# Kernel tuning notes

Hardware: AMD Instinct MI355X
Metric: run time of the kernel (lower is better)

## Reference

```python
import jax, jax.numpy as jnp
import numpy as np

B, Q, C, H, D, E, I = 8, 256, 192, 20, 64, 1500, 5120
HID = H * D  # 1280
EPS = 1e-5
SCALE = D ** -0.5


def _linear(x, w, b):
    return jnp.einsum('bsh,oh->bso', x, w) + b


def _layernorm(x, w, b):
    xf = x.astype(jnp.float32)
    mu = jnp.mean(xf, axis=-1, keepdims=True)
    var = jnp.mean(jnp.square(xf - mu), axis=-1, keepdims=True)
    return ((xf - mu) * jax.lax.rsqrt(var + EPS) * w + b).astype(x.dtype)


def _heads(x):  # [B,S,HID] -> [B,H,S,D]
    return x.reshape(B, -1, H, D).transpose(0, 2, 1, 3)


def setup_inputs() -> dict:
    key = jax.random.key(0)
    ks = jax.random.split(key, 24)
    s = 0.02
    inp = {
        'hidden_states': jax.random.normal(ks[0], (B, Q, HID), jnp.float32),
        'mask': jnp.zeros((B, 1, Q, Q + C), jnp.float32),
        'past_key': jax.random.normal(ks[1], (B, H, C, D), jnp.float32),
        'past_value': jax.random.normal(ks[2], (B, H, C, D), jnp.float32),
        'cross_key': jax.random.normal(ks[3], (B, H, E, D), jnp.float32),
        'cross_value': jax.random.normal(ks[4], (B, H, E, D), jnp.float32),
        'q_w': jax.random.normal(ks[5], (HID, HID), jnp.float32) * s,
        'q_b': jnp.zeros((HID,), jnp.float32),
        'k_w': jax.random.normal(ks[6], (HID, HID), jnp.float32) * s,
        'k_b': jnp.zeros((HID,), jnp.float32),
        'v_w': jax.random.normal(ks[7], (HID, HID), jnp.float32) * s,
        'v_b': jnp.zeros((HID,), jnp.float32),
        'o_w': jax.random.normal(ks[8], (HID, HID), jnp.float32) * s,
        'o_b': jnp.zeros((HID,), jnp.float32),
        'cq_w': jax.random.normal(ks[9], (HID, HID), jnp.float32) * s,
        'cq_b': jnp.zeros((HID,), jnp.float32),
        'co_w': jax.random.normal(ks[10], (HID, HID), jnp.float32) * s,
        'co_b': jnp.zeros((HID,), jnp.float32),
        'up_w': jax.random.normal(ks[11], (I, HID), jnp.float32) * s,
        'up_b': jnp.zeros((I,), jnp.float32),
        'down_w': jax.random.normal(ks[12], (HID, I), jnp.float32) * s,
        'down_b': jnp.zeros((HID,), jnp.float32),
        'ln1_w': jnp.ones((HID,), jnp.float32),
        'ln1_b': jnp.zeros((HID,), jnp.float32),
        'ln2_w': jnp.ones((HID,), jnp.float32),
        'ln2_b': jnp.zeros((HID,), jnp.float32),
        'ln3_w': jnp.ones((HID,), jnp.float32),
        'ln3_b': jnp.zeros((HID,), jnp.float32),
    }
    return inp


def reference(hidden_states, mask, past_key, past_value, cross_key, cross_value,
              q_w, q_b, k_w, k_b, v_w, v_b, o_w, o_b,
              cq_w, cq_b, co_w, co_b, up_w, up_b, down_w, down_b,
              ln1_w, ln1_b, ln2_w, ln2_b, ln3_w, ln3_b):
    # ---- self-attention block ----
    residual = hidden_states
    x = _layernorm(hidden_states, ln1_w, ln1_b)
    q = _heads(_linear(x, q_w, q_b) * SCALE)          # [B,H,Q,D]
    k_new = _heads(_linear(x, k_w, k_b))              # [B,H,Q,D]
    v_new = _heads(_linear(x, v_w, v_b))
    k = jnp.concatenate([past_key, k_new], axis=2)    # [B,H,C+Q,D]
    v = jnp.concatenate([past_value, v_new], axis=2)
    scores = jnp.einsum('bhqd,bhkd->bhqk', q, k) + mask
    attn = jnp.einsum('bhqk,bhkd->bhqd', jax.nn.softmax(scores, axis=-1), v)
    attn = attn.transpose(0, 2, 1, 3).reshape(B, Q, HID)
    attn_out = _linear(attn, o_w, o_b)
    present_key = k[:, :, Q:, :]
    present_value = v[:, :, Q:, :]
    h = residual + attn_out
    # ---- cross-attention block ----
    residual = h
    x = _layernorm(h, ln2_w, ln2_b)
    cq = _heads(_linear(x, cq_w, cq_b) * SCALE)       # [B,H,Q,D]
    cscores = jnp.einsum('bhqd,bhkd->bhqk', cq, cross_key)
    cattn = jnp.einsum('bhqk,bhkd->bhqd', jax.nn.softmax(cscores, axis=-1), cross_value)
    cattn = cattn.transpose(0, 2, 1, 3).reshape(B, Q, HID)
    h = residual + _linear(cattn, co_w, co_b)
    # ---- MLP block ----
    residual = h
    x = _layernorm(h, ln3_w, ln3_b)
    up = _linear(x, up_w, up_b)
    mlp_out = _linear(jax.nn.gelu(up, approximate=False), down_w, down_b)
    h = residual + mlp_out
    return (h, present_key, present_value)
```

## Files before the change

kernel.cpp:

```cpp
#include <hip/hip_runtime.h>
#include <math.h>

#define Bc   8
#define Qn   256
#define Cn   192
#define Hn   20
#define Dn   64
#define En   1500
#define In   5120
#define HIDn 1280
#define BQ   2048
#define KSELF 448
#define EPAD 1536
#define S1   (BQ*HIDn)
#define WSZ  (HIDn*HIDn)
#define BH   (Bc*Hn)

typedef __attribute__((ext_vector_type(8))) short bf16x8;
typedef __attribute__((ext_vector_type(4))) float f32x4;

__device__ __forceinline__ short f2bf(float f) {
  union { float f; unsigned u; } x; x.f = f;
  unsigned r = x.u + 0x7fffu + ((x.u >> 16) & 1u);
  return (short)(r >> 16);
}
__device__ __forceinline__ float bf2f(short s) {
  union { unsigned u; float f; } x; x.u = ((unsigned)(unsigned short)s) << 16;
  return x.f;
}
__device__ __forceinline__ void gload16(const short* g, short* l) {
  __builtin_amdgcn_global_load_lds(
      (const __attribute__((address_space(1))) void*)g,
      (__attribute__((address_space(3))) void*)l, 16, 0, 0);
}
__device__ __forceinline__ bf16x8 cvt8(const float* p) {
  const float4 a = *reinterpret_cast<const float4*>(p);
  const float4 b = *reinterpret_cast<const float4*>(p + 4);
  bf16x8 t;
  t[0] = f2bf(a.x); t[1] = f2bf(a.y); t[2] = f2bf(a.z); t[3] = f2bf(a.w);
  t[4] = f2bf(b.x); t[5] = f2bf(b.y); t[6] = f2bf(b.z); t[7] = f2bf(b.w);
  return t;
}

__global__ __launch_bounds__(256) void convert_all(
    const float* q, const float* k, const float* v, const float* o,
    const float* cq, const float* co, const float* up, const float* dn,
    short* wq, short* wk, short* wv, short* wo,
    short* wcq, short* wco, short* wup, short* wdn)
{
  const float* src; short* dst; int n;
  switch (blockIdx.y) {
    case 0: src = q;  dst = wq;  n = WSZ; break;
    case 1: src = k;  dst = wk;  n = WSZ; break;
    case 2: src = v;  dst = wv;  n = WSZ; break;
    case 3: src = o;  dst = wo;  n = WSZ; break;
    case 4: src = cq; dst = wcq; n = WSZ; break;
    case 5: src = co; dst = wco; n = WSZ; break;
    case 6: src = up; dst = wup; n = HIDn * In; break;
    default: src = dn; dst = wdn; n = HIDn * In; break;
  }
  const int i = (blockIdx.x * 256 + threadIdx.x) * 8;
  if (i >= n) return;
  *reinterpret_cast<bf16x8*>(dst + i) = cvt8(src + i);
}

__global__ __launch_bounds__(256) void prep_cross(
    const float* __restrict__ K, const float* __restrict__ V,
    short* __restrict__ Kc, short* __restrict__ Vc)
{
  const size_t idx = (size_t)blockIdx.x * 256 + threadIdx.x;
  const int d8 = (int)(idx & 7) * 8;
  const size_t t = idx >> 3;
  const int key = (int)(t % EPAD);
  const int bh  = (int)(t / EPAD);
  bf16x8 kv = (bf16x8)0, vv = (bf16x8)0;
  if (key < En) {
    const size_t off = ((size_t)bh * En + key) * 64 + d8;
    kv = cvt8(K + off);
    vv = cvt8(V + off);
  }
  const size_t dst = ((size_t)bh * EPAD + key) * 64 + d8;
  *reinterpret_cast<bf16x8*>(Kc + dst) = kv;
  *reinterpret_cast<bf16x8*>(Vc + dst) = vv;
}

__global__ __launch_bounds__(256) void prep_self(
    const float* __restrict__ Kp, const float* __restrict__ Vp,
    const short* __restrict__ kn, const short* __restrict__ vn,
    short* __restrict__ Kc, short* __restrict__ Vc)
{
  const size_t idx = (size_t)blockIdx.x * 256 + threadIdx.x;
  const int d8 = (int)(idx & 7) * 8;
  const size_t t = idx >> 3;
  const int key = (int)(t % KSELF);
  const int bh  = (int)(t / KSELF);
  bf16x8 kv, vv;
  if (key < Cn) {
    const size_t off = ((size_t)bh * Cn + key) * 64 + d8;
    kv = cvt8(Kp + off);
    vv = cvt8(Vp + off);
  } else {
    const int b = bh / Hn, h = bh % Hn;
    const size_t off = ((size_t)(b * Qn + (key - Cn))) * HIDn + h * 64 + d8;
    kv = *reinterpret_cast<const bf16x8*>(kn + off);
    vv = *reinterpret_cast<const bf16x8*>(vn + off);
  }
  const size_t dst = ((size_t)bh * KSELF + key) * 64 + d8;
  *reinterpret_cast<bf16x8*>(Kc + dst) = kv;
  *reinterpret_cast<bf16x8*>(Vc + dst) = vv;
}

template<bool BFIN>
__global__ __launch_bounds__(256) void layernorm_k(
    const void* __restrict__ in, const float* __restrict__ w,
    const float* __restrict__ b, short* __restrict__ out)
{
  const int row = blockIdx.x;
  float v[5], s = 0.f, s2 = 0.f;
#pragma unroll
  for (int i = 0; i < 5; ++i) {
    const int c = threadIdx.x + 256 * i;
    float t;
    if (BFIN) t = bf2f(((const short*)in)[(size_t)row * HIDn + c]);
    else      t = ((const float*)in)[(size_t)row * HIDn + c];
    v[i] = t; s += t; s2 += t * t;
  }
#pragma unroll
  for (int off = 1; off < 64; off <<= 1) {
    s  += __shfl_xor(s,  off, 64);
    s2 += __shfl_xor(s2, off, 64);
  }
  __shared__ float red[8];
  const int wave = threadIdx.x >> 6, lane = threadIdx.x & 63;
  if (lane == 0) { red[wave] = s; red[wave + 4] = s2; }
  __syncthreads();
  s  = red[0] + red[1] + red[2] + red[3];
  s2 = red[4] + red[5] + red[6] + red[7];
  const float mu  = s / HIDn;
  const float var = s2 / HIDn - mu * mu;
  const float rs  = rsqrtf(var + 1e-5f);
#pragma unroll
  for (int i = 0; i < 5; ++i) {
    const int c = threadIdx.x + 256 * i;
    out[(size_t)row * HIDn + c] = f2bf((v[i] - mu) * rs * w[c] + b[c]);
  }
}

template<int BM, int BN, int MODE>
__global__ __launch_bounds__(256) void gemm_db(
    const short* __restrict__ A, const short* __restrict__ W,
    const float* __restrict__ bias, const void* __restrict__ resid,
    void* __restrict__ out0, void* __restrict__ out1, void* __restrict__ out2,
    const float* __restrict__ b1, const float* __restrict__ b2,
    int N, int K, int LDK, float scale)
{
  constexpr int FM = BM / 32, FN = BN / 32;
  constexpr int ASH = BM * 64, BSH = BN * 64;
  __shared__ __align__(16) short smem[2 * ASH + 2 * BSH];
  const int tid = threadIdx.x, lane = tid & 63, wave = tid >> 6;
  const int wr = wave >> 1, wc = wave & 1;
  const int lr = lane & 15;
  const int kc = (lane >> 4) * 8;

  const int GX = gridDim.x, T = GX * gridDim.y;
  int orig = blockIdx.x + GX * blockIdx.y;
  const int cpx = T >> 3;
  const int lid = (orig & 7) * cpx + (orig >> 3);
  const int m0 = (lid % GX) * BM;
  const int n0 = (lid / GX) * BN;

  f32x4 acc[FM][FN];
#pragma unroll
  for (int mi = 0; mi < FM; ++mi)
#pragma unroll
    for (int ni = 0; ni < FN; ++ni)
      acc[mi][ni] = (f32x4){0.f, 0.f, 0.f, 0.f};

  auto STAGE = [&](int kt, int buf) {
    const int k0 = kt << 6;
#pragma unroll
    for (int j = 0; j < BM / 32; ++j) {
      const int i = wave + 4 * j;
      const int rr = i >> 1, kk = i & 1;
      gload16(A + (size_t)(m0 + rr * 16 + lr) * LDK + k0 + kk * 32 + kc,
              &smem[buf * ASH + i * 512]);
    }
#pragma unroll
    for (int j = 0; j < BN / 32; ++j) {
      const int i = wave + 4 * j;
      const int rr = i >> 1, kk = i & 1;
      gload16(W + (size_t)(n0 + rr * 16 + lr) * LDK + k0 + kk * 32 + kc,
              &smem[2 * ASH + buf * BSH + i * 512]);
    }
  };

  const int nk = K >> 6;
  STAGE(0, 0);
  asm volatile("s_waitcnt vmcnt(0)" ::: "memory");
  __builtin_amdgcn_s_barrier();
  __builtin_amdgcn_sched_barrier(0);

  int cur = 0;
  for (int kt = 0; kt < nk; ++kt) {
    if (kt + 1 < nk) STAGE(kt + 1, cur ^ 1);
    bf16x8 af[2][FM], bfv[2][FN];
#pragma unroll
    for (int kk = 0; kk < 2; ++kk) {
#pragma unroll
      for (int mi = 0; mi < FM; ++mi)
        af[kk][mi] = *reinterpret_cast<const bf16x8*>(
            &smem[cur * ASH + ((wr * FM + mi) * 2 + kk) * 512 + lane * 8]);
#pragma unroll
      for (int ni = 0; ni < FN; ++ni)
        bfv[kk][ni] = *reinterpret_cast<const bf16x8*>(
            &smem[2 * ASH + cur * BSH + ((wc * FN + ni) * 2 + kk) * 512 + lane * 8]);
    }
#pragma unroll
    for (int kk = 0; kk < 2; ++kk)
#pragma unroll
      for (int mi = 0; mi < FM; ++mi)
#pragma unroll
        for (int ni = 0; ni < FN; ++ni)
          acc[mi][ni] = __builtin_amdgcn_mfma_f32_16x16x32_bf16(
              af[kk][mi], bfv[kk][ni], acc[mi][ni], 0, 0, 0);
    __builtin_amdgcn_sched_barrier(0);
    asm volatile("s_waitcnt vmcnt(0)" ::: "memory");
    __builtin_amdgcn_s_barrier();
    __builtin_amdgcn_sched_barrier(0);
    cur ^= 1;
  }

  __syncthreads();
  float* ep = (float*)smem;
  constexpr int PS = BN + 4;
  constexpr int halfM = BM / 2;
  const int cn = lane & 15;
  const int rb = (lane >> 4) * 4;
  const int rg = (MODE == 3) ? n0 / 1280 : 0;
  const float* bp = (MODE == 3) ? (rg == 0 ? bias : rg == 1 ? b1 : b2) : bias;
  const float  sc = (MODE == 3) ? (rg == 0 ? 0.125f : 1.f) : scale;
  short* op3 = (MODE == 3)
      ? (rg == 0 ? (short*)out0 : rg == 1 ? (short*)out1 : (short*)out2) : nullptr;

#pragma unroll
  for (int p = 0; p < BM / 32; ++p) {
    if (wr == (p * 32) / halfM) {
      const int mi0 = ((p * 32) % halfM) / 16;
#pragma unroll
      for (int mm = 0; mm < 2; ++mm)
#pragma unroll
        for (int ni = 0; ni < FN; ++ni)
#pragma unroll
          for (int j = 0; j < 4; ++j)
            ep[(mm * 16 + rb + j) * PS + wc * (BN / 2) + ni * 16 + cn] =
                acc[mi0 + mm][ni][j];
    }
    __syncthreads();
#pragma unroll
    for (int c = 0; c < 32 * BN / 8 / 256; ++c) {
      const int ci = tid + c * 256;
      const int r  = ci / (BN / 8);
      const int c8 = (ci % (BN / 8)) * 8;
      const int grow = m0 + p * 32 + r;
      const int gcol = n0 + c8;
      float f[8];
#pragma unroll
      for (int i = 0; i < 4; ++i) f[i] = ep[r * PS + c8 + i];
#pragma unroll
      for (int i = 0; i < 4; ++i) f[4 + i] = ep[r * PS + c8 + 4 + i];
      const float4 bv0 = *reinterpret_cast<const float4*>(bp + (MODE == 3 ? gcol - rg * 1280 : gcol));
      const float4 bv1 = *reinterpret_cast<const float4*>(bp + (MODE == 3 ? gcol - rg * 1280 : gcol) + 4);
      const float bb[8] = {bv0.x, bv0.y, bv0.z, bv0.w, bv1.x, bv1.y, bv1.z, bv1.w};
#pragma unroll
      for (int i = 0; i < 8; ++i) f[i] += bb[i];
      if (MODE == 0) {
        const float* rp = (const float*)resid + (size_t)grow * N + gcol;
        float4 o0, o1;
        const float4 r0 = *reinterpret_cast<const float4*>(rp);
        const float4 r1 = *reinterpret_cast<const float4*>(rp + 4);
        o0.x = f[0] + r0.x; o0.y = f[1] + r0.y; o0.z = f[2] + r0.z; o0.w = f[3] + r0.w;
        o1.x = f[4] + r1.x; o1.y = f[5] + r1.y; o1.z = f[6] + r1.z; o1.w = f[7] + r1.w;
        float* outp = (float*)out0 + (size_t)grow * N + gcol;
        *reinterpret_cast<float4*>(outp) = o0;
        *reinterpret_cast<float4*>(outp + 4) = o1;
      } else if (MODE == 6) {
        const bf16x8 rv = *reinterpret_cast<const bf16x8*>((const short*)resid + (size_t)grow * N + gcol);
        float4 o0, o1;
        o0.x = f[0] + bf2f(rv[0]); o0.y = f[1] + bf2f(rv[1]);
        o0.z = f[2] + bf2f(rv[2]); o0.w = f[3] + bf2f(rv[3]);
        o1.x = f[4] + bf2f(rv[4]); o1.y = f[5] + bf2f(rv[5]);
        o1.z = f[6] + bf2f(rv[6]); o1.w = f[7] + bf2f(rv[7]);
        float* outp = (float*)out0 + (size_t)grow * N + gcol;
        *reinterpret_cast<float4*>(outp) = o0;
        *reinterpret_cast<float4*>(outp + 4) = o1;
      } else if (MODE == 5) {
        const float* rp = (const float*)resid + (size_t)grow * N + gcol;
        const float4 r0 = *reinterpret_cast<const float4*>(rp);
        const float4 r1 = *reinterpret_cast<const float4*>(rp + 4);
        const float rr[8] = {r0.x, r0.y, r0.z, r0.w, r1.x, r1.y, r1.z, r1.w};
        bf16x8 o;
#pragma unroll
        for (int i = 0; i < 8; ++i) o[i] = f2bf(f[i] + rr[i]);
        *reinterpret_cast<bf16x8*>((short*)out0 + (size_t)grow * N + gcol) = o;
      } else if (MODE == 1) {
        bf16x8 o;
#pragma unroll
        for (int i = 0; i < 8; ++i) o[i] = f2bf(f[i] * sc);
        *reinterpret_cast<bf16x8*>((short*)out0 + (size_t)grow * N + gcol) = o;
      } else if (MODE == 2) {
        bf16x8 o;
#pragma unroll
        for (int i = 0; i < 8; ++i) {
          const float t = f[i];
          o[i] = f2bf(0.5f * t * (1.f + erff(t * 0.70710678118654752f)));
        }
        *reinterpret_cast<bf16x8*>((short*)out0 + (size_t)grow * N + gcol) = o;
      } else {
        bf16x8 o;
#pragma unroll
        for (int i = 0; i < 8; ++i) o[i] = f2bf(f[i] * sc);
        *reinterpret_cast<bf16x8*>(op3 + (size_t)grow * 1280 + (gcol - rg * 1280)) = o;
      }
    }
    __syncthreads();
  }
}

template<bool HASMASK>
__global__ __launch_bounds__(256) void attn_mfma(
    const short* __restrict__ Qb, const short* __restrict__ Kc,
    const short* __restrict__ Vc, const float* __restrict__ mask,
    short* __restrict__ Ob, int PADK, int KT)
{
  const int orig = blockIdx.x;
  const int idx  = (orig & 7) * 80 + (orig >> 3);
  const int qt = idx & 3;
  const int h  = (idx >> 2) % Hn;
  const int b  = idx / (4 * Hn);
  const int bh = b * Hn + h;
  const int tid = threadIdx.x, lane = tid & 63, wave = tid >> 6;
  const int q0 = qt * 64;
  const int cn = lane & 15;
  const int hg = lane >> 4;
  const int rb = hg * 4;

  __shared__ __align__(16) short k_s[64][72];
  __shared__ __align__(16) short vt_s[64][72];
  __shared__ __align__(16) short p_s[4][16][72];

  bf16x8 aq[2];
  {
    const short* qrow = Qb + (size_t)(b * Qn + q0 + wave * 16 + cn) * HIDn + h * 64;
    aq[0] = *reinterpret_cast<const bf16x8*>(qrow + hg * 8);
    aq[1] = *reinterpret_cast<const bf16x8*>(qrow + 32 + hg * 8);
  }

  float mrun[4] = {-1e30f, -1e30f, -1e30f, -1e30f};
  float lrun[4] = {0.f, 0.f, 0.f, 0.f};
  f32x4 oacc[4];
#pragma unroll
  for (int t = 0; t < 4; ++t) oacc[t] = (f32x4){0.f, 0.f, 0.f, 0.f};

  const int nchunk = PADK >> 6;
  for (int ci = 0; ci < nchunk; ++ci) {
    const int c0 = ci * 64;
    const short* kbase = Kc + ((size_t)bh * PADK + c0) * 64;
    const short* vbase = Vc + ((size_t)bh * PADK + c0) * 64;
#pragma unroll
    for (int r = 0; r < 2; ++r) {
      const int i = tid + r * 256;
      const int key = i >> 3, d8 = (i & 7) * 8;
      const bf16x8 kv = *reinterpret_cast<const bf16x8*>(kbase + key * 64 + d8);
      const bf16x8 vv = *reinterpret_cast<const bf16x8*>(vbase + key * 64 + d8);
      *reinterpret_cast<bf16x8*>(&k_s[key][d8]) = kv;
      const int g = key >> 3, o = key & 7, f = i & 7;
      const int col = ((g ^ f) << 3) | o;
#pragma unroll
      for (int j = 0; j < 8; ++j) vt_s[d8 + j][col] = vv[j];
    }
    __syncthreads();

    f32x4 sacc[4];
#pragma unroll
    for (int t = 0; t < 4; ++t) sacc[t] = (f32x4){0.f, 0.f, 0.f, 0.f};
#pragma unroll
    for (int t = 0; t < 4; ++t)
#pragma unroll
      for (int kk = 0; kk < 2; ++kk) {
        const bf16x8 bk = *reinterpret_cast<const bf16x8*>(&k_s[t * 16 + cn][kk * 32 + hg * 8]);
        sacc[t] = __builtin_amdgcn_mfma_f32_16x16x32_bf16(aq[kk], bk, sacc[t], 0, 0, 0);
      }

    float sc[4][4];
#pragma unroll
    for (int t = 0; t < 4; ++t) {
      const int key = c0 + t * 16 + cn;
      const bool valid = key < KT;
#pragma unroll
      for (int j = 0; j < 4; ++j) {
        float v = sacc[t][j];
        if (HASMASK && valid)
          v += mask[((size_t)(b * Qn) + q0 + wave * 16 + rb + j) * KT + key];
        sc[t][j] = valid ? v : -1e30f;
      }
    }

#pragma unroll
    for (int j = 0; j < 4; ++j) {
      float mx = fmaxf(fmaxf(sc[0][j], sc[1][j]), fmaxf(sc[2][j], sc[3][j]));
#pragma unroll
      for (int off = 1; off < 16; off <<= 1) mx = fmaxf(mx, __shfl_xor(mx, off, 64));
      if (mx > mrun[j] + 8.f) {
        const float alpha = __expf(mrun[j] - mx);
        lrun[j] *= alpha;
#pragma unroll
        for (int t = 0; t < 4; ++t) oacc[t][j] *= alpha;
        mrun[j] = mx;
      }
      float ps = 0.f;
#pragma unroll
      for (int t = 0; t < 4; ++t) {
        const float p = __expf(sc[t][j] - mrun[j]);
        sc[t][j] = p; ps += p;
      }
#pragma unroll
      for (int off = 1; off < 16; off <<= 1) ps += __shfl_xor(ps, off, 64);
      lrun[j] += ps;
    }

#pragma unroll
    for (int t = 0; t < 4; ++t)
#pragma unroll
      for (int j = 0; j < 4; ++j)
        p_s[wave][rb + j][t * 16 + cn] = f2bf(sc[t][j]);

    const bf16x8 ap0 = *reinterpret_cast<const bf16x8*>(&p_s[wave][cn][hg * 8]);
    const bf16x8 ap1 = *reinterpret_cast<const bf16x8*>(&p_s[wave][cn][32 + hg * 8]);
#pragma unroll
    for (int t = 0; t < 4; ++t) {
      const int d  = t * 16 + cn;
      const int fd = (d >> 3) & 7;
      const bf16x8 bv0 = *reinterpret_cast<const bf16x8*>(&vt_s[d][((hg)     ^ fd) << 3]);
      const bf16x8 bv1 = *reinterpret_cast<const bf16x8*>(&vt_s[d][((4 + hg) ^ fd) << 3]);
      oacc[t] = __builtin_amdgcn_mfma_f32_16x16x32_bf16(ap0, bv0, oacc[t], 0, 0, 0);
      oacc[t] = __builtin_amdgcn_mfma_f32_16x16x32_bf16(ap1, bv1, oacc[t], 0, 0, 0);
    }
    __syncthreads();
  }

#pragma unroll
  for (int t = 0; t < 4; ++t)
#pragma unroll
    for (int j = 0; j < 4; ++j)
      Ob[(size_t)(b * Qn + q0 + wave * 16 + rb + j) * HIDn + h * 64 + t * 16 + cn] =
          f2bf(oacc[t][j] / lrun[j]);
}

__global__ __launch_bounds__(256) void copy_present(
    const short* __restrict__ kn, const short* __restrict__ vn,
    float* __restrict__ outk, float* __restrict__ outv)
{
  const int idx = blockIdx.x * 256 + threadIdx.x;
  if (idx >= Bc * Hn * Cn * 8) return;
  const int d8 = (idx & 7) * 8;
  int t = idx >> 3;
  const int c = t % Cn; t /= Cn;
  const int h = t % Hn;
  const int b = t / Hn;
  const size_t src = (size_t)(b * Qn + (Qn - Cn) + c) * HIDn + h * 64 + d8;
  const size_t dst = (((size_t)b * Hn + h) * Cn + c) * 64 + d8;
  const bf16x8 kv = *reinterpret_cast<const bf16x8*>(kn + src);
  const bf16x8 vv = *reinterpret_cast<const bf16x8*>(vn + src);
#pragma unroll
  for (int j = 0; j < 8; ++j) {
    outk[dst + j] = bf2f(kv[j]);
    outv[dst + j] = bf2f(vv[j]);
  }
}

extern "C" void kernel_launch(void* const* d_in, const int* in_sizes, int n_in,
                              void* d_out, int out_size, void* d_ws, size_t ws_size,
                              hipStream_t stream)
{
  const float* hidden  = (const float*)d_in[0];
  const float* mask    = (const float*)d_in[1];
  const float* past_k  = (const float*)d_in[2];
  const float* past_v  = (const float*)d_in[3];
  const float* cross_k = (const float*)d_in[4];
  const float* cross_v = (const float*)d_in[5];
  const float* q_w  = (const float*)d_in[6];  const float* q_b  = (const float*)d_in[7];
  const float* k_w  = (const float*)d_in[8];  const float* k_b  = (const float*)d_in[9];
  const float* v_w  = (const float*)d_in[10]; const float* v_b  = (const float*)d_in[11];
  const float* o_w  = (const float*)d_in[12]; const float* o_b  = (const float*)d_in[13];
  const float* cq_w = (const float*)d_in[14]; const float* cq_b = (const float*)d_in[15];
  const float* co_w = (const float*)d_in[16]; const float* co_b = (const float*)d_in[17];
  const float* up_w = (const float*)d_in[18]; const float* up_b = (const float*)d_in[19];
  const float* dn_w = (const float*)d_in[20]; const float* dn_b = (const float*)d_in[21];
  const float* ln1w = (const float*)d_in[22]; const float* ln1b = (const float*)d_in[23];
  const float* ln2w = (const float*)d_in[24]; const float* ln2b = (const float*)d_in[25];
  const float* ln3w = (const float*)d_in[26]; const float* ln3b = (const float*)d_in[27];

  short* wq  = (short*)d_ws;
  short* wk  = wq  + (size_t)WSZ;
  short* wv  = wk  + (size_t)WSZ;
  short* wo  = wv  + (size_t)WSZ;
  short* wcq = wo  + (size_t)WSZ;
  short* wco = wcq + (size_t)WSZ;
  short* wup = wco + (size_t)WSZ;
  short* wdn = wup + (size_t)HIDn * In;
  short* xb  = wdn + (size_t)HIDn * In;
  short* qb  = xb  + (size_t)S1;
  short* kb  = qb  + (size_t)S1;
  short* vb  = kb  + (size_t)S1;
  short* ab  = vb  + (size_t)S1;
  short* U   = ab  + (size_t)S1;
  short* ksb = U;
  short* vsb = U + (size_t)BH * KSELF * 64;
  short* upa = U;
  short* kcc = U + (size_t)BQ * In;
  short* vcc = kcc + (size_t)BH * EPAD * 64;
  short* h1b = (short*)(vcc + (size_t)BH * EPAD * 64);

  float* out_h  = (float*)d_out;
  float* out_pk = out_h + (size_t)S1;
  float* out_pv = out_pk + (size_t)(Bc * Hn * Cn * Dn);
  float* h2 = out_h;

  const dim3 blk(256);
  const dim3 gconv(3200, 8);
  const dim3 gqkv(16, 30);
  const dim3 gn64(16, 20);
  const dim3 gup(16, 40);
  const dim3 gattn(640);

  convert_all<<<gconv, blk, 0, stream>>>(q_w, k_w, v_w, o_w, cq_w, co_w, up_w, dn_w,
                                         wq, wk, wv, wo, wcq, wco, wup, wdn);
  prep_cross<<<(BH * EPAD * 8) / 256, blk, 0, stream>>>(cross_k, cross_v, kcc, vcc);
  layernorm_k<false><<<BQ, blk, 0, stream>>>(hidden, ln1w, ln1b, xb);
  gemm_db<128, 128, 3><<<gqkv, blk, 0, stream>>>(xb, wq, q_b, nullptr,
      qb, kb, vb, k_b, v_b, 3840, HIDn, HIDn, 1.f);
  copy_present<<<(Bc * Hn * Cn * 8 + 255) / 256, blk, 0, stream>>>(kb, vb, out_pk, out_pv);
  prep_self<<<(BH * KSELF * 8) / 256, blk, 0, stream>>>(past_k, past_v, kb, vb, ksb, vsb);
  attn_mfma<true><<<gattn, blk, 0, stream>>>(qb, ksb, vsb, mask, ab, KSELF, KSELF);
  gemm_db<128, 64, 5><<<gn64, blk, 0, stream>>>(ab, wo, o_b, hidden,
      h1b, nullptr, nullptr, nullptr, nullptr, HIDn, HIDn, HIDn, 1.f);
  layernorm_k<true><<<BQ, blk, 0, stream>>>(h1b, ln2w, ln2b, xb);
  gemm_db<128, 64, 1><<<gn64, blk, 0, stream>>>(xb, wcq, cq_b, nullptr,
      qb, nullptr, nullptr, nullptr, nullptr, HIDn, HIDn, HIDn, 0.125f);
  attn_mfma<false><<<gattn, blk, 0, stream>>>(qb, kcc, vcc, nullptr, ab, EPAD, En);
  gemm_db<128, 64, 6><<<gn64, blk, 0, stream>>>(ab, wco, co_b, h1b,
      h2, nullptr, nullptr, nullptr, nullptr, HIDn, HIDn, HIDn, 1.f);
  layernorm_k<false><<<BQ, blk, 0, stream>>>(h2, ln3w, ln3b, xb);
  gemm_db<128, 128, 2><<<gup, blk, 0, stream>>>(xb, wup, up_b, nullptr,
      upa, nullptr, nullptr, nullptr, nullptr, In, HIDn, HIDn, 1.f);
  gemm_db<128, 64, 0><<<gn64, blk, 0, stream>>>(upa, wdn, dn_b, h2,
      out_h, nullptr, nullptr, nullptr, nullptr, HIDn, In, In, 1.f);
}
```

Measured before the change: 566.0 us.

## Use 8-wave blocks for GEMMs and attention, direct-store epilogue

The GEMMs move to 512-thread blocks with a 2x4 wave grid, and the N-width-1280 GEMMs change tile shape from 128x64 to 64x128. The LDS-staged coalesced epilogue is replaced by direct per-element scalar stores from accumulators. Attention blocks now cover 128 queries with 8 waves, which halves the grid and shares each K/V chunk load across twice as many queries. This trades some occupancy and store coalescing for more MFMA work per staged tile and fewer synchronisations.

Measured after the change: 550.4 us. -2.8%, faster.

```diff
diff --git a/kernel.cpp b/kernel.cpp
--- a/kernel.cpp
+++ b/kernel.cpp
@@ -147,23 +147,25 @@
 }
 
 template<int BM, int BN, int MODE>
-__global__ __launch_bounds__(256) void gemm_db(
+__global__ __launch_bounds__(512) void gemm8(
     const short* __restrict__ A, const short* __restrict__ W,
     const float* __restrict__ bias, const void* __restrict__ resid,
     void* __restrict__ out0, void* __restrict__ out1, void* __restrict__ out2,
     const float* __restrict__ b1, const float* __restrict__ b2,
     int N, int K, int LDK, float scale)
 {
-  constexpr int FM = BM / 32, FN = BN / 32;
+  constexpr int FM = BM / 32, FN = BN / 64;
+  constexpr int NLA = BM / 64, NLB = BN / 64;
   constexpr int ASH = BM * 64, BSH = BN * 64;
-  __shared__ __align__(16) short smem[2 * ASH + 2 * BSH];
+  __shared__ __align__(16) short Alds[2][ASH];
+  __shared__ __align__(16) short Blds[2][BSH];
   const int tid = threadIdx.x, lane = tid & 63, wave = tid >> 6;
-  const int wr = wave >> 1, wc = wave & 1;
+  const int wm = wave >> 2, wn = wave & 3;
   const int lr = lane & 15;
   const int kc = (lane >> 4) * 8;
 
   const int GX = gridDim.x, T = GX * gridDim.y;
-  int orig = blockIdx.x + GX * blockIdx.y;
+  const int orig = blockIdx.x + GX * blockIdx.y;
   const int cpx = T >> 3;
   const int lid = (orig & 7) * cpx + (orig >> 3);
   const int m0 = (lid % GX) * BM;
@@ -179,18 +181,18 @@
   auto STAGE = [&](int kt, int buf) {
     const int k0 = kt << 6;
 #pragma unroll
-    for (int j = 0; j < BM / 32; ++j) {
-      const int i = wave + 4 * j;
+    for (int j = 0; j < NLA; ++j) {
+      const int i = wave + 8 * j;
       const int rr = i >> 1, kk = i & 1;
       gload16(A + (size_t)(m0 + rr * 16 + lr) * LDK + k0 + kk * 32 + kc,
-              &smem[buf * ASH + i * 512]);
-    }
-#pragma unroll
-    for (int j = 0; j < BN / 32; ++j) {
-      const int i = wave + 4 * j;
+              &Alds[buf][i * 512]);
+    }
+#pragma unroll
+    for (int j = 0; j < NLB; ++j) {
+      const int i = wave + 8 * j;
       const int rr = i >> 1, kk = i & 1;
       gload16(W + (size_t)(n0 + rr * 16 + lr) * LDK + k0 + kk * 32 + kc,
-              &smem[2 * ASH + buf * BSH + i * 512]);
+              &Blds[buf][i * 512]);
     }
   };
 
@@ -209,11 +211,11 @@
 #pragma unroll
       for (int mi = 0; mi < FM; ++mi)
         af[kk][mi] = *reinterpret_cast<const bf16x8*>(
-            &smem[cur * ASH + ((wr * FM + mi) * 2 + kk) * 512 + lane * 8]);
+            &Alds[cur][((wm * FM + mi) * 2 + kk) * 512 + lane * 8]);
 #pragma unroll
       for (int ni = 0; ni < FN; ++ni)
         bfv[kk][ni] = *reinterpret_cast<const bf16x8*>(
-            &smem[2 * ASH + cur * BSH + ((wc * FN + ni) * 2 + kk) * 512 + lane * 8]);
+            &Blds[cur][((wn * FN + ni) * 2 + kk) * 512 + lane * 8]);
     }
 #pragma unroll
     for (int kk = 0; kk < 2; ++kk)
@@ -230,10 +232,6 @@
     cur ^= 1;
   }
 
-  __syncthreads();
-  float* ep = (float*)smem;
-  constexpr int PS = BN + 4;
-  constexpr int halfM = BM / 2;
   const int cn = lane & 15;
   const int rb = (lane >> 4) * 4;
   const int rg = (MODE == 3) ? n0 / 1280 : 0;
@@ -241,112 +239,58 @@
   const float  sc = (MODE == 3) ? (rg == 0 ? 0.125f : 1.f) : scale;
   short* op3 = (MODE == 3)
       ? (rg == 0 ? (short*)out0 : rg == 1 ? (short*)out1 : (short*)out2) : nullptr;
-
-#pragma unroll
-  for (int p = 0; p < BM / 32; ++p) {
-    if (wr == (p * 32) / halfM) {
-      const int mi0 = ((p * 32) % halfM) / 16;
-#pragma unroll
-      for (int mm = 0; mm < 2; ++mm)
-#pragma unroll
-        for (int ni = 0; ni < FN; ++ni)
-#pragma unroll
-          for (int j = 0; j < 4; ++j)
-            ep[(mm * 16 + rb + j) * PS + wc * (BN / 2) + ni * 16 + cn] =
-                acc[mi0 + mm][ni][j];
-    }
-    __syncthreads();
-#pragma unroll
-    for (int c = 0; c < 32 * BN / 8 / 256; ++c) {
-      const int ci = tid + c * 256;
-      const int r  = ci / (BN / 8);
-      const int c8 = (ci % (BN / 8)) * 8;
-      const int grow = m0 + p * 32 + r;
-      const int gcol = n0 + c8;
-      float f[8];
-#pragma unroll
-      for (int i = 0; i < 4; ++i) f[i] = ep[r * PS + c8 + i];
-#pragma unroll
-      for (int i = 0; i < 4; ++i) f[4 + i] = ep[r * PS + c8 + 4 + i];
-      const float4 bv0 = *reinterpret_cast<const float4*>(bp + (MODE == 3 ? gcol - rg * 1280 : gcol));
-      const float4 bv1 = *reinterpret_cast<const float4*>(bp + (MODE == 3 ? gcol - rg * 1280 : gcol) + 4);
-      const float bb[8] = {bv0.x, bv0.y, bv0.z, bv0.w, bv1.x, bv1.y, bv1.z, bv1.w};
-#pragma unroll
-      for (int i = 0; i < 8; ++i) f[i] += bb[i];
-      if (MODE == 0) {
-        const float* rp = (const float*)resid + (size_t)grow * N + gcol;
-        float4 o0, o1;
-        const float4 r0 = *reinterpret_cast<const float4*>(rp);
-        const float4 r1 = *reinterpret_cast<const float4*>(rp + 4);
-        o0.x = f[0] + r0.x; o0.y = f[1] + r0.y; o0.z = f[2] + r0.z; o0.w = f[3] + r0.w;
-        o1.x = f[4] + r1.x; o1.y = f[5] + r1.y; o1.z = f[6] + r1.z; o1.w = f[7] + r1.w;
-        float* outp = (float*)out0 + (size_t)grow * N + gcol;
-        *reinterpret_cast<float4*>(outp) = o0;
-        *reinterpret_cast<float4*>(outp + 4) = o1;
-      } else if (MODE == 6) {
-        const bf16x8 rv = *reinterpret_cast<const bf16x8*>((const short*)resid + (size_t)grow * N + gcol);
-        float4 o0, o1;
-        o0.x = f[0] + bf2f(rv[0]); o0.y = f[1] + bf2f(rv[1]);
-        o0.z = f[2] + bf2f(rv[2]); o0.w = f[3] + bf2f(rv[3]);
-        o1.x = f[4] + bf2f(rv[4]); o1.y = f[5] + bf2f(rv[5]);
-        o1.z = f[6] + bf2f(rv[6]); o1.w = f[7] + bf2f(rv[7]);
-        float* outp = (float*)out0 + (size_t)grow * N + gcol;
-        *reinterpret_cast<float4*>(outp) = o0;
-        *reinterpret_cast<float4*>(outp + 4) = o1;
-      } else if (MODE == 5) {
-        const float* rp = (const float*)resid + (size_t)grow * N + gcol;
-        const float4 r0 = *reinterpret_cast<const float4*>(rp);
-        const float4 r1 = *reinterpret_cast<const float4*>(rp + 4);
-        const float rr[8] = {r0.x, r0.y, r0.z, r0.w, r1.x, r1.y, r1.z, r1.w};
-        bf16x8 o;
-#pragma unroll
-        for (int i = 0; i < 8; ++i) o[i] = f2bf(f[i] + rr[i]);
-        *reinterpret_cast<bf16x8*>((short*)out0 + (size_t)grow * N + gcol) = o;
-      } else if (MODE == 1) {
-        bf16x8 o;
-#pragma unroll
-        for (int i = 0; i < 8; ++i) o[i] = f2bf(f[i] * sc);
-        *reinterpret_cast<bf16x8*>((short*)out0 + (size_t)grow * N + gcol) = o;
-      } else if (MODE == 2) {
-        bf16x8 o;
-#pragma unroll
-        for (int i = 0; i < 8; ++i) {
-          const float t = f[i];
-          o[i] = f2bf(0.5f * t * (1.f + erff(t * 0.70710678118654752f)));
+#pragma unroll
+  for (int mi = 0; mi < FM; ++mi)
+#pragma unroll
+    for (int ni = 0; ni < FN; ++ni)
+#pragma unroll
+      for (int j = 0; j < 4; ++j) {
+        const int row = m0 + wm * (BM / 2) + mi * 16 + rb + j;
+        const int col = n0 + wn * (BN / 4) + ni * 16 + cn;
+        const float a = acc[mi][ni][j];
+        if (MODE == 0) {
+          ((float*)out0)[(size_t)row * N + col] =
+              a + bp[col] + ((const float*)resid)[(size_t)row * N + col];
+        } else if (MODE == 6) {
+          ((float*)out0)[(size_t)row * N + col] =
+              a + bp[col] + bf2f(((const short*)resid)[(size_t)row * N + col]);
+        } else if (MODE == 5) {
+          ((short*)out0)[(size_t)row * N + col] =
+              f2bf(a + bp[col] + ((const float*)resid)[(size_t)row * N + col]);
+        } else if (MODE == 1) {
+          ((short*)out0)[(size_t)row * N + col] = f2bf((a + bp[col]) * sc);
+        } else if (MODE == 2) {
+          float t = a + bp[col];
+          t = 0.5f * t * (1.f + erff(t * 0.70710678118654752f));
+          ((short*)out0)[(size_t)row * N + col] = f2bf(t);
+        } else {
+          const int cl = col - rg * 1280;
+          op3[(size_t)row * 1280 + cl] = f2bf((a + bp[cl]) * sc);
         }
-        *reinterpret_cast<bf16x8*>((short*)out0 + (size_t)grow * N + gcol) = o;
-      } else {
-        bf16x8 o;
-#pragma unroll
-        for (int i = 0; i < 8; ++i) o[i] = f2bf(f[i] * sc);
-        *reinterpret_cast<bf16x8*>(op3 + (size_t)grow * 1280 + (gcol - rg * 1280)) = o;
       }
-    }
-    __syncthreads();
-  }
 }
 
 template<bool HASMASK>
-__global__ __launch_bounds__(256) void attn_mfma(
+__global__ __launch_bounds__(512) void attn_mfma(
     const short* __restrict__ Qb, const short* __restrict__ Kc,
     const short* __restrict__ Vc, const float* __restrict__ mask,
     short* __restrict__ Ob, int PADK, int KT)
 {
   const int orig = blockIdx.x;
-  const int idx  = (orig & 7) * 80 + (orig >> 3);
-  const int qt = idx & 3;
-  const int h  = (idx >> 2) % Hn;
-  const int b  = idx / (4 * Hn);
+  const int idx  = (orig & 7) * 40 + (orig >> 3);
+  const int qt = idx & 1;
+  const int h  = (idx >> 1) % Hn;
+  const int b  = idx / (2 * Hn);
   const int bh = b * Hn + h;
   const int tid = threadIdx.x, lane = tid & 63, wave = tid >> 6;
-  const int q0 = qt * 64;
+  const int q0 = qt * 128;
   const int cn = lane & 15;
   const int hg = lane >> 4;
   const int rb = hg * 4;
 
   __shared__ __align__(16) short k_s[64][72];
   __shared__ __align__(16) short vt_s[64][72];
-  __shared__ __align__(16) short p_s[4][16][72];
+  __shared__ __align__(16) short p_s[8][16][72];
 
   bf16x8 aq[2];
   {
@@ -366,9 +310,8 @@
     const int c0 = ci * 64;
     const short* kbase = Kc + ((size_t)bh * PADK + c0) * 64;
     const short* vbase = Vc + ((size_t)bh * PADK + c0) * 64;
-#pragma unroll
-    for (int r = 0; r < 2; ++r) {
-      const int i = tid + r * 256;
+    {
+      const int i = tid;
       const int key = i >> 3, d8 = (i & 7) * 8;
       const bf16x8 kv = *reinterpret_cast<const bf16x8*>(kbase + key * 64 + d8);
       const bf16x8 vv = *reinterpret_cast<const bf16x8*>(vbase + key * 64 + d8);
@@ -527,32 +470,33 @@
   float* h2 = out_h;
 
   const dim3 blk(256);
+  const dim3 blk8(512);
   const dim3 gconv(3200, 8);
   const dim3 gqkv(16, 30);
-  const dim3 gn64(16, 20);
+  const dim3 gn64(32, 10);
   const dim3 gup(16, 40);
-  const dim3 gattn(640);
+  const dim3 gattn(320);
 
   convert_all<<<gconv, blk, 0, stream>>>(q_w, k_w, v_w, o_w, cq_w, co_w, up_w, dn_w,
                                          wq, wk, wv, wo, wcq, wco, wup, wdn);
   prep_cross<<<(BH * EPAD * 8) / 256, blk, 0, stream>>>(cross_k, cross_v, kcc, vcc);
   layernorm_k<false><<<BQ, blk, 0, stream>>>(hidden, ln1w, ln1b, xb);
-  gemm_db<128, 128, 3><<<gqkv, blk, 0, stream>>>(xb, wq, q_b, nullptr,
+  gemm8<128, 128, 3><<<gqkv, blk8, 0, stream>>>(xb, wq, q_b, nullptr,
       qb, kb, vb, k_b, v_b, 3840, HIDn, HIDn, 1.f);
   copy_present<<<(Bc * Hn * Cn * 8 + 255) / 256, blk, 0, stream>>>(kb, vb, out_pk, out_pv);
   prep_self<<<(BH * KSELF * 8) / 256, blk, 0, stream>>>(past_k, past_v, kb, vb, ksb, vsb);
-  attn_mfma<true><<<gattn, blk, 0, stream>>>(qb, ksb, vsb, mask, ab, KSELF, KSELF);
-  gemm_db<128, 64, 5><<<gn64, blk, 0, stream>>>(ab, wo, o_b, hidden,
+  attn_mfma<true><<<gattn, blk8, 0, stream>>>(qb, ksb, vsb, mask, ab, KSELF, KSELF);
+  gemm8<64, 128, 5><<<gn64, blk8, 0, stream>>>(ab, wo, o_b, hidden,
       h1b, nullptr, nullptr, nullptr, nullptr, HIDn, HIDn, HIDn, 1.f);
   layernorm_k<true><<<BQ, blk, 0, stream>>>(h1b, ln2w, ln2b, xb);
-  gemm_db<128, 64, 1><<<gn64, blk, 0, stream>>>(xb, wcq, cq_b, nullptr,
+  gemm8<64, 128, 1><<<gn64, blk8, 0, stream>>>(xb, wcq, cq_b, nullptr,
       qb, nullptr, nullptr, nullptr, nullptr, HIDn, HIDn, HIDn, 0.125f);
-  attn_mfma<false><<<gattn, blk, 0, stream>>>(qb, kcc, vcc, nullptr, ab, EPAD, En);
-  gemm_db<128, 64, 6><<<gn64, blk, 0, stream>>>(ab, wco, co_b, h1b,
+  attn_mfma<false><<<gattn, blk8, 0, stream>>>(qb, kcc, vcc, nullptr, ab, EPAD, En);
+  gemm8<64, 128, 6><<<gn64, blk8, 0, stream>>>(ab, wco, co_b, h1b,
       h2, nullptr, nullptr, nullptr, nullptr, HIDn, HIDn, HIDn, 1.f);
   layernorm_k<false><<<BQ, blk, 0, stream>>>(h2, ln3w, ln3b, xb);
-  gemm_db<128, 128, 2><<<gup, blk, 0, stream>>>(xb, wup, up_b, nullptr,
+  gemm8<128, 128, 2><<<gup, blk8, 0, stream>>>(xb, wup, up_b, nullptr,
       upa, nullptr, nullptr, nullptr, nullptr, In, HIDn, HIDn, 1.f);
-  gemm_db<128, 64, 0><<<gn64, blk, 0, stream>>>(upa, wdn, dn_b, h2,
+  gemm8<64, 128, 0><<<gn64, blk8, 0, stream>>>(upa, wdn, dn_b, h2,
       out_h, nullptr, nullptr, nullptr, nullptr, HIDn, In, In, 1.f);
 }
```
